# Performance work log

Hardware: AMD Instinct MI355X
Metric: run time of the kernel (lower is better)

Reference implementation:

```python
import jax, jax.numpy as jnp
import numpy as np

BETA = 5.0
NEG = jnp.float32(-1e30)  # finite stand-in for -inf; avoids NaN on the fully-masked row 0


def setup_inputs() -> dict:
    key = jax.random.key(0)
    ks = jax.random.split(key, 6)
    B, L, d, dv, dh = 4, 4096, 512, 512, 512
    K = jax.random.normal(ks[0], (B, L, d), dtype=jnp.float32)
    V = jax.random.normal(ks[1], (B, L, dv), dtype=jnp.float32)
    # nn.Linear weights: shape (out, in), applied as x @ W.T
    Wq = jax.random.normal(ks[2], (dh, d), dtype=jnp.float32) / np.sqrt(d).astype(np.float32)
    Wk = jax.random.normal(ks[3], (dh, d), dtype=jnp.float32) / np.sqrt(d).astype(np.float32)
    Wv = jax.random.normal(ks[4], (dv, dv), dtype=jnp.float32) / np.sqrt(dv).astype(np.float32)
    Wo = jax.random.normal(ks[5], (dv, dv), dtype=jnp.float32) / np.sqrt(dv).astype(np.float32)
    return {"K": K, "V": V, "Wq": Wq, "Wk": Wk, "Wv": Wv, "Wo": Wo}


def reference(K, V, Wq, Wk, Wv, Wo):
    B, L, _ = K.shape
    dh = Wq.shape[0]
    Qh = jnp.einsum('bld,hd->blh', K, Wq)
    Kh = jnp.einsum('bld,hd->blh', K, Wk)
    Vp = jnp.einsum('bld,ed->ble', V, Wv)
    scale = jnp.float32(BETA) / jnp.sqrt(jnp.float32(dh))
    scores = jnp.einsum('bih,bjh->bij', Qh, Kh) * scale  # [B,L,L]
    # strict causal mask: attend only to j <= i-1 (triu with diagonal=0 masked)
    mask = jnp.triu(jnp.ones((L, L), dtype=bool), k=0)
    scores = jnp.where(mask[None], NEG, scores)
    attn = jax.nn.softmax(scores, axis=-1)
    # row 0 has no past: torch code zeroes it after softmax
    attn = attn.at[:, 0, :].set(0.0)
    out = jnp.einsum('bij,bjd->bid', attn, Vp)
    Vhat = jnp.einsum('bld,ed->ble', out, Wo)
    return Vhat
```

## Files before the change

kernel.cpp:

```cpp
#include <hip/hip_runtime.h>


typedef unsigned short u16;
typedef _Float16 f16;
typedef short short8 __attribute__((ext_vector_type(8)));
typedef _Float16 half8 __attribute__((ext_vector_type(8)));
typedef _Float16 half4 __attribute__((ext_vector_type(4)));
typedef float floatx4 __attribute__((ext_vector_type(4)));

#define L_SEQ 4096
#define NBATCH 4
#define DMODEL 512
#define SCALE 0.22097086912079612f
#define MMAX 30.0f

__device__ __forceinline__ u16 f2bf(float f) {
  unsigned int u = __float_as_uint(f);
  u += 0x7fffu + ((u >> 16) & 1u);
  return (u16)(u >> 16);
}
__device__ __forceinline__ float bf2f(u16 h) {
  return __uint_as_float(((unsigned int)h) << 16);
}

__device__ __forceinline__ void gl2lds16(const void* g, void* l) {
  __builtin_amdgcn_global_load_lds(
      (const __attribute__((address_space(1))) unsigned int*)g,
      (__attribute__((address_space(3))) unsigned int*)l, 16, 0, 0);
}

__global__ __launch_bounds__(256) void cvt_f16v(const float4* __restrict__ x,
                                                half4* __restrict__ o, int n4) {
  int i = blockIdx.x * 256 + threadIdx.x;
  if (i >= n4) return;
  float4 f = x[i];
  half4 h = {(f16)f.x, (f16)f.y, (f16)f.z, (f16)f.w};
  o[i] = h;
}

template <int OUT_MODE>
__global__ __launch_bounds__(256, 2) void gemm128(
    const f16* __restrict__ A, const f16* __restrict__ B,
    void* __restrict__ Cout, int ldc, long sAz, long sBz, long sCz) {
  __shared__ f16 sA[128 * 64];
  __shared__ f16 sB[128 * 64];

  const int tid = threadIdx.x;
  const int wave = tid >> 6, lane = tid & 63, quad = lane >> 4, l16 = lane & 15;
  const int wm = (wave >> 1) * 64, wn = (wave & 1) * 64;
  const int bn = blockIdx.x * 128, bm = blockIdx.y * 128, bz = blockIdx.z;

  const f16* Ab = A + (long)bz * sAz + (long)bm * 512;
  const f16* Bb = B + (long)bz * sBz + (long)bn * 512;

  floatx4 zero = {0.f, 0.f, 0.f, 0.f};
  floatx4 acc[4][4];
#pragma unroll
  for (int mi = 0; mi < 4; mi++)
#pragma unroll
    for (int ni = 0; ni < 4; ni++) acc[mi][ni] = zero;

  const int lrow = lane >> 3;
  for (int ks = 0; ks < 8; ks++) {
    __syncthreads();
#pragma unroll
    for (int i = 0; i < 4; i++) {
      int r0 = wave * 32 + i * 8;
      int r = r0 + lrow;
      int c = ((lane & 7) - r) & 7;
      gl2lds16(Ab + (long)r * 512 + ks * 64 + c * 8, &sA[r0 * 64]);
      gl2lds16(Bb + (long)r * 512 + ks * 64 + c * 8, &sB[r0 * 64]);
    }
    __syncthreads();
#pragma unroll
    for (int kk = 0; kk < 2; kk++) {
      half8 af[4], bf[4];
#pragma unroll
      for (int mi = 0; mi < 4; mi++) {
        int row = wm + mi * 16 + l16;
        int slot = (kk * 4 + quad + row) & 7;
        af[mi] = *(const half8*)&sA[row * 64 + slot * 8];
      }
#pragma unroll
      for (int ni = 0; ni < 4; ni++) {
        int row = wn + ni * 16 + l16;
        int slot = (kk * 4 + quad + row) & 7;
        bf[ni] = *(const half8*)&sB[row * 64 + slot * 8];
      }
#pragma unroll
      for (int mi = 0; mi < 4; mi++)
#pragma unroll
        for (int ni = 0; ni < 4; ni++)
          acc[mi][ni] = __builtin_amdgcn_mfma_f32_16x16x32_f16(
              af[mi], bf[ni], acc[mi][ni], 0, 0, 0);
    }
  }

#pragma unroll
  for (int mi = 0; mi < 4; mi++) {
#pragma unroll
    for (int ni = 0; ni < 4; ni++) {
#pragma unroll
      for (int rr = 0; rr < 4; rr++) {
        int row = bm + wm + mi * 16 + quad * 4 + rr;
        int col = bn + wn + ni * 16 + l16;
        long idx = (long)bz * sCz + (long)row * ldc + col;
        float v = acc[mi][ni][rr];
        if (OUT_MODE == 1) {
          ((f16*)Cout)[idx] = (f16)v;
        } else if (OUT_MODE == 3) {
          ((u16*)Cout)[idx] = f2bf(v);
        } else {
          ((float*)Cout)[idx] = v;
        }
      }
    }
  }
}

__device__ __forceinline__ int nseg_of(int qt) {
  return (qt < 12) ? ((qt + 2) >> 1) : ((qt + 4) >> 2);
}
__device__ __forceinline__ int seg_off(int qt) {
  int o = 0;
  for (int q = 2; q < qt; q++) o += 4 * nseg_of(q);
  return o;
}

#define SV_LD 40

__global__ __launch_bounds__(512, 2) void attn_kernel(
    const f16* __restrict__ Qh_g, const f16* __restrict__ Kh_g,
    const u16* __restrict__ VpT, f16* __restrict__ Ob,
    u16* __restrict__ Opart, float* __restrict__ ml) {
  __shared__ f16 sK[2][32 * 512];
  __shared__ u16 sV[2][512 * 32];
  __shared__ u16 sP[8 * 16 * SV_LD];
  __shared__ float sL[128];

  const int tid = threadIdx.x;
  const int wave = tid >> 6, lane = tid & 63, quad = lane >> 4, l16 = lane & 15;

  int id = blockIdx.x;
  int qt = 31;
  for (;;) {
    int c = 4 * nseg_of(qt);
    if (id < c) break;
    id -= c;
    qt--;
  }
  const int S = nseg_of(qt);
  const int b = id / S;
  const int s = id - b * S;
  const int ktn = 4 * qt + 4;
  const int base = ktn / S, rem = ktn - base * S;
  const int len = base + (s < rem);
  const int start = s * base + (s < rem ? s : rem);

  const int q0 = qt * 128 + wave * 16;
  const long qbase = (long)b * L_SEQ + q0;

  half8 qf[16];
#pragma unroll
  for (int c = 0; c < 16; c++) {
    long a = (qbase + l16) * 512 + c * 32 + quad * 8;
    qf[c] = *(const half8*)&Qh_g[a];
  }

  floatx4 zero = {0.f, 0.f, 0.f, 0.f};
  float l_run[4] = {0.f, 0.f, 0.f, 0.f};
  floatx4 oacc[32];
#pragma unroll
  for (int nb = 0; nb < 32; nb++) oacc[nb] = zero;

  const f16* __restrict__ Kh_b = Kh_g + (long)b * L_SEQ * 512;
  const u16* __restrict__ V_b  = VpT + (long)b * (512L * L_SEQ);

  auto stage = [&](int bs, int jt) {
    const int j0 = jt * 32;
#pragma unroll
    for (int i = 0; i < 4; i++) {
      int r = wave * 4 + i;
      int k = (lane - (r & 7)) & 63;
      gl2lds16(Kh_b + (long)(j0 + r) * 512 + k * 8, &sK[bs][r * 512]);
    }
#pragma unroll
    for (int i = 0; i < 4; i++) {
      int g = wave * 4 + i;
      int d = g * 16 + (lane >> 2);
      int c = ((lane & 3) - d) & 3;
      gl2lds16(V_b + (long)d * L_SEQ + j0 + c * 8, &sV[bs][g * 512]);
    }
  };

  stage(0, start);

  for (int v = 0; v < len; v++) {
    const int j0 = (start + v) * 32;
    const int cur = v & 1;

    __syncthreads();
    if (v + 1 < len) stage(cur ^ 1, start + v + 1);

    const f16* kc = &sK[cur][0];
    const u16* vc = &sV[cur][0];

    floatx4 sacc0 = zero, sacc1 = zero;
    const int rot = l16 & 7;
#pragma unroll
    for (int c = 0; c < 16; c++) {
      int slot = (c * 4 + quad + rot) & 63;
      half8 b0 = *(const half8*)&kc[l16 * 512 + slot * 8];
      half8 b1 = *(const half8*)&kc[(16 + l16) * 512 + slot * 8];
      sacc0 = __builtin_amdgcn_mfma_f32_16x16x32_f16(qf[c], b0, sacc0, 0, 0, 0);
      sacc1 = __builtin_amdgcn_mfma_f32_16x16x32_f16(qf[c], b1, sacc1, 0, 0, 0);
    }

#pragma unroll
    for (int rr = 0; rr < 4; rr++) {
      int irow = q0 + quad * 4 + rr;
      float s0 = fmaf(sacc0[rr], SCALE, -MMAX);
      float s1 = fmaf(sacc1[rr], SCALE, -MMAX);
      if (j0 + l16 >= irow) s0 = -1e30f;
      if (j0 + 16 + l16 >= irow) s1 = -1e30f;
      float p0 = __expf(s0);
      float p1 = __expf(s1);
      l_run[rr] += p0 + p1;
      int pb = wave * (16 * SV_LD) + (quad * 4 + rr) * SV_LD;
      sP[pb + l16] = f2bf(p0);
      sP[pb + 16 + l16] = f2bf(p1);
    }

    __builtin_amdgcn_sched_barrier(0);
    __builtin_amdgcn_s_waitcnt(0xC07F);
    __builtin_amdgcn_s_barrier();
    __builtin_amdgcn_sched_barrier(0);

    short8 vf[4];
#pragma unroll
    for (int nbl = 0; nbl < 4; nbl++) {
      int dvr = wave * 64 + nbl * 16 + l16;
      vf[nbl] = *(const short8*)&vc[dvr * 32 + ((quad + l16) & 3) * 8];
    }
#pragma unroll
    for (int qg = 0; qg < 8; qg++) {
      short8 ap = *(const short8*)&sP[qg * (16 * SV_LD) + l16 * SV_LD + quad * 8];
#pragma unroll
      for (int nbl = 0; nbl < 4; nbl++)
        oacc[qg * 4 + nbl] =
            __builtin_amdgcn_mfma_f32_16x16x32_bf16(ap, vf[nbl], oacc[qg * 4 + nbl], 0, 0, 0);
    }
  }

#pragma unroll
  for (int rr = 0; rr < 4; rr++) {
    float l = l_run[rr];
    l += __shfl_xor(l, 1);
    l += __shfl_xor(l, 2);
    l += __shfl_xor(l, 4);
    l += __shfl_xor(l, 8);
    l_run[rr] = l;
  }
  if (l16 == 0) {
#pragma unroll
    for (int rr = 0; rr < 4; rr++) sL[wave * 16 + quad * 4 + rr] = l_run[rr];
  }
  __syncthreads();

  if (S == 1) {
#pragma unroll
    for (int qg = 0; qg < 8; qg++) {
#pragma unroll
      for (int rr = 0; rr < 4; rr++) {
        int row = qg * 16 + quad * 4 + rr;
        int irow = qt * 128 + row;
        float lv = sL[row];
        float inv = (irow == 0 || lv <= 0.f) ? 0.f : 1.0f / lv;
        long obase = ((long)b * L_SEQ + irow) * 512 + wave * 64;
#pragma unroll
        for (int nbl = 0; nbl < 4; nbl++)
          Ob[obase + nbl * 16 + l16] = (f16)(oacc[qg * 4 + nbl][rr] * inv);
      }
    }
  } else {
    const int slot = seg_off(qt) + b * S + s;
    const long obase0 = (long)slot * (128 * 512);
#pragma unroll
    for (int qg = 0; qg < 8; qg++) {
#pragma unroll
      for (int rr = 0; rr < 4; rr++) {
        int row = qg * 16 + quad * 4 + rr;
        long ob = obase0 + (long)row * 512 + wave * 64;
#pragma unroll
        for (int nbl = 0; nbl < 4; nbl++)
          Opart[ob + nbl * 16 + l16] = f2bf(oacc[qg * 4 + nbl][rr]);
      }
    }
    if (l16 == 0) {
#pragma unroll
      for (int rr = 0; rr < 4; rr++)
        ml[slot * 128 + wave * 16 + quad * 4 + rr] = l_run[rr];
    }
  }
}

__global__ __launch_bounds__(256) void attn_combine(
    const u16* __restrict__ Opart, const float* __restrict__ ml,
    f16* __restrict__ Ob) {
  const int qt = 2 + (blockIdx.x >> 2), b = blockIdx.x & 3;
  const int S = nseg_of(qt);
  const int bslot = seg_off(qt) + b * S;
  __shared__ float sInv[128];
  const int tid = threadIdx.x;
  if (tid < 128) {
    int row = tid, irow = qt * 128 + row;
    float ltot = 0.f;
    for (int s = 0; s < S; s++) ltot += ml[(bslot + s) * 128 + row];
    sInv[row] = (irow == 0 || ltot <= 0.f) ? 0.f : 1.0f / ltot;
  }
  __syncthreads();
  const int c0 = blockIdx.y * 16;
  for (int idx = tid; idx < 128 * 16; idx += 256) {
    int row = idx >> 4, cc = c0 + (idx & 15);
    float acc[8] = {0, 0, 0, 0, 0, 0, 0, 0};
    for (int s = 0; s < S; s++) {
      int4 pk = *(const int4*)&Opart[(long)(bslot + s) * 65536 + row * 512 + cc * 8];
      const u16* ph = (const u16*)&pk;
#pragma unroll
      for (int e = 0; e < 8; e++) acc[e] += bf2f(ph[e]);
    }
    float inv = sInv[row];
    f16 o[8];
#pragma unroll
    for (int e = 0; e < 8; e++) o[e] = (f16)(acc[e] * inv);
    *(int4*)&Ob[((long)b * L_SEQ + qt * 128 + row) * 512 + cc * 8] = *(int4*)o;
  }
}

extern "C" void kernel_launch(void* const* d_in, const int* in_sizes, int n_in,
                              void* d_out, int out_size, void* d_ws, size_t ws_size,
                              hipStream_t stream) {
  const float* K  = (const float*)d_in[0];
  const float* V  = (const float*)d_in[1];
  const float* Wq = (const float*)d_in[2];
  const float* Wk = (const float*)d_in[3];
  const float* Wv = (const float*)d_in[4];
  const float* Wo = (const float*)d_in[5];
  float* out = (float*)d_out;

  const int NKV = NBATCH * L_SEQ * DMODEL;
  const int NW = DMODEL * DMODEL;
  const int NSLOT = 640;

  char* w = (char*)d_ws;
  size_t off = 0;
  auto carve = [&](size_t bytes) {
    void* p = w + off;
    off += (bytes + 255) & ~(size_t)255;
    return p;
  };
  f16* Qh   = (f16*)carve((size_t)NKV * 2);
  f16* Kh   = (f16*)carve((size_t)NKV * 2);
  u16* VpTw = (u16*)carve((size_t)NKV * 2);
  f16* Obw  = (f16*)carve((size_t)NKV * 2);
  f16* Wo16 = (f16*)carve((size_t)NW * 2);
  float* mlw = (float*)carve((size_t)NSLOT * 128 * 4);
  u16* Opart = (u16*)carve((size_t)NSLOT * 65536 * 2);
  f16* K16  = (f16*)Opart;
  f16* V16  = K16 + NKV;
  f16* Wq16 = V16 + NKV;
  f16* Wk16 = Wq16 + NW;
  f16* Wv16 = Wk16 + NW;

  cvt_f16v<<<NKV / 1024, 256, 0, stream>>>((const float4*)K, (half4*)K16, NKV / 4);
  cvt_f16v<<<NKV / 1024, 256, 0, stream>>>((const float4*)V, (half4*)V16, NKV / 4);
  cvt_f16v<<<NW / 1024, 256, 0, stream>>>((const float4*)Wq, (half4*)Wq16, NW / 4);
  cvt_f16v<<<NW / 1024, 256, 0, stream>>>((const float4*)Wk, (half4*)Wk16, NW / 4);
  cvt_f16v<<<NW / 1024, 256, 0, stream>>>((const float4*)Wv, (half4*)Wv16, NW / 4);
  cvt_f16v<<<NW / 1024, 256, 0, stream>>>((const float4*)Wo, (half4*)Wo16, NW / 4);

  gemm128<1><<<dim3(4, 128, 1), 256, 0, stream>>>(
      K16, Wq16, (void*)Qh, 512, 0, 0, 0);
  gemm128<1><<<dim3(4, 128, 1), 256, 0, stream>>>(
      K16, Wk16, (void*)Kh, 512, 0, 0, 0);

  gemm128<3><<<dim3(32, 4, NBATCH), 256, 0, stream>>>(
      Wv16, V16, (void*)VpTw, L_SEQ, 0, (long)L_SEQ * 512, (long)512 * L_SEQ);

  attn_kernel<<<dim3(648, 1, 1), 512, 0, stream>>>(
      Qh, Kh, VpTw, Obw, Opart, mlw);
  attn_combine<<<dim3(120, 4, 1), 256, 0, stream>>>(Opart, mlw, Obw);

  gemm128<2><<<dim3(4, 128, 1), 256, 0, stream>>>(
      Obw, Wo16, (void*)out, 512, 0, 0, 0);

  (void)in_sizes; (void)n_in; (void)out_size; (void)ws_size;
}
```

Baseline: 358.2 us.

## Double KV tile to 64 and load V fragments directly from global

Widens the key tile from 32 to 64 rows per iteration, halving the number of barriers and loop trips per block. V is no longer staged through LDS; each wave loads its V fragments straight from global memory into registers, one half before the softmax and one half after the barrier. This frees LDS for the larger K double buffer but exposes global-load latency in the PV stage and raises register pressure, which may limit occupancy at two blocks per CU.

```diff
diff --git a/kernel.cpp b/kernel.cpp
--- a/kernel.cpp
+++ b/kernel.cpp
@@ -127,15 +127,14 @@
   return o;
 }
 
-#define SV_LD 40
+#define SP_LD 72
 
 __global__ __launch_bounds__(512, 2) void attn_kernel(
     const f16* __restrict__ Qh_g, const f16* __restrict__ Kh_g,
     const u16* __restrict__ VpT, f16* __restrict__ Ob,
     u16* __restrict__ Opart, float* __restrict__ ml) {
-  __shared__ f16 sK[2][32 * 512];
-  __shared__ u16 sV[2][512 * 32];
-  __shared__ u16 sP[8 * 16 * SV_LD];
+  __shared__ f16 sK[2][64 * 512];
+  __shared__ u16 sP[8 * 16 * SP_LD];
   __shared__ float sL[128];
 
   const int tid = threadIdx.x;
@@ -152,7 +151,7 @@
   const int S = nseg_of(qt);
   const int b = id / S;
   const int s = id - b * S;
-  const int ktn = 4 * qt + 4;
+  const int ktn = 2 * qt + 2;
   const int base = ktn / S, rem = ktn - base * S;
   const int len = base + (s < rem);
   const int start = s * base + (s < rem ? s : rem);
@@ -177,58 +176,59 @@
   const u16* __restrict__ V_b  = VpT + (long)b * (512L * L_SEQ);
 
   auto stage = [&](int bs, int jt) {
-    const int j0 = jt * 32;
-#pragma unroll
-    for (int i = 0; i < 4; i++) {
-      int r = wave * 4 + i;
+    const int j0 = jt * 64;
+#pragma unroll
+    for (int i = 0; i < 8; i++) {
+      int r = wave * 8 + i;
       int k = (lane - (r & 7)) & 63;
       gl2lds16(Kh_b + (long)(j0 + r) * 512 + k * 8, &sK[bs][r * 512]);
     }
-#pragma unroll
-    for (int i = 0; i < 4; i++) {
-      int g = wave * 4 + i;
-      int d = g * 16 + (lane >> 2);
-      int c = ((lane & 3) - d) & 3;
-      gl2lds16(V_b + (long)d * L_SEQ + j0 + c * 8, &sV[bs][g * 512]);
-    }
   };
 
   stage(0, start);
 
   for (int v = 0; v < len; v++) {
-    const int j0 = (start + v) * 32;
+    const int j0 = (start + v) * 64;
     const int cur = v & 1;
 
     __syncthreads();
     if (v + 1 < len) stage(cur ^ 1, start + v + 1);
 
     const f16* kc = &sK[cur][0];
-    const u16* vc = &sV[cur][0];
-
-    floatx4 sacc0 = zero, sacc1 = zero;
+
+    floatx4 sacc[4] = {zero, zero, zero, zero};
     const int rot = l16 & 7;
 #pragma unroll
     for (int c = 0; c < 16; c++) {
       int slot = (c * 4 + quad + rot) & 63;
-      half8 b0 = *(const half8*)&kc[l16 * 512 + slot * 8];
-      half8 b1 = *(const half8*)&kc[(16 + l16) * 512 + slot * 8];
-      sacc0 = __builtin_amdgcn_mfma_f32_16x16x32_f16(qf[c], b0, sacc0, 0, 0, 0);
-      sacc1 = __builtin_amdgcn_mfma_f32_16x16x32_f16(qf[c], b1, sacc1, 0, 0, 0);
+#pragma unroll
+      for (int t = 0; t < 4; t++) {
+        half8 bt = *(const half8*)&kc[(t * 16 + l16) * 512 + slot * 8];
+        sacc[t] = __builtin_amdgcn_mfma_f32_16x16x32_f16(qf[c], bt, sacc[t], 0, 0, 0);
+      }
+    }
+
+    short8 vf0[4];
+#pragma unroll
+    for (int nbl = 0; nbl < 4; nbl++) {
+      long dvr = wave * 64 + nbl * 16 + l16;
+      vf0[nbl] = *(const short8*)&V_b[dvr * L_SEQ + j0 + quad * 8];
     }
 
 #pragma unroll
     for (int rr = 0; rr < 4; rr++) {
       int irow = q0 + quad * 4 + rr;
-      float s0 = fmaf(sacc0[rr], SCALE, -MMAX);
-      float s1 = fmaf(sacc1[rr], SCALE, -MMAX);
-      if (j0 + l16 >= irow) s0 = -1e30f;
-      if (j0 + 16 + l16 >= irow) s1 = -1e30f;
-      float p0 = __expf(s0);
-      float p1 = __expf(s1);
-      l_run[rr] += p0 + p1;
-      int pb = wave * (16 * SV_LD) + (quad * 4 + rr) * SV_LD;
-      sP[pb + l16] = f2bf(p0);
-      sP[pb + 16 + l16] = f2bf(p1);
+      int pb = wave * (16 * SP_LD) + (quad * 4 + rr) * SP_LD;
+      float lacc = 0.f;
+#pragma unroll
+      for (int t = 0; t < 4; t++) {
+        float st = fmaf(sacc[t][rr], SCALE, -MMAX);
+        if (j0 + t * 16 + l16 >= irow) st = -1e30f;
+        float p = __expf(st);
+        lacc += p;
+        sP[pb + t * 16 + l16] = f2bf(p);
+      }
+      l_run[rr] += lacc;
     }
 
     __builtin_amdgcn_sched_barrier(0);
@@ -236,19 +236,27 @@
     __builtin_amdgcn_s_barrier();
     __builtin_amdgcn_sched_barrier(0);
 
-    short8 vf[4];
+    short8 vf1[4];
 #pragma unroll
     for (int nbl = 0; nbl < 4; nbl++) {
-      int dvr = wave * 64 + nbl * 16 + l16;
-      vf[nbl] = *(const short8*)&vc[dvr * 32 + ((quad + l16) & 3) * 8];
+      long dvr = wave * 64 + nbl * 16 + l16;
+      vf1[nbl] = *(const short8*)&V_b[dvr * L_SEQ + j0 + 32 + quad * 8];
     }
 #pragma unroll
     for (int qg = 0; qg < 8; qg++) {
-      short8 ap = *(const short8*)&sP[qg * (16 * SV_LD) + l16 * SV_LD + quad * 8];
+      short8 ap = *(const short8*)&sP[qg * (16 * SP_LD) + l16 * SP_LD + quad * 8];
 #pragma unroll
       for (int nbl = 0; nbl < 4; nbl++)
         oacc[qg * 4 + nbl] =
-            __builtin_amdgcn_mfma_f32_16x16x32_bf16(ap, vf[nbl], oacc[qg * 4 + nbl], 0, 0, 0);
+            __builtin_amdgcn_mfma_f32_16x16x32_bf16(ap, vf0[nbl], oacc[qg * 4 + nbl], 0, 0, 0);
+    }
+#pragma unroll
+    for (int qg = 0; qg < 8; qg++) {
+      short8 ap = *(const short8*)&sP[qg * (16 * SP_LD) + l16 * SP_LD + 32 + quad * 8];
+#pragma unroll
+      for (int nbl = 0; nbl < 4; nbl++)
+        oacc[qg * 4 + nbl] =
+            __builtin_amdgcn_mfma_f32_16x16x32_bf16(ap, vf1[nbl], oacc[qg * 4 + nbl], 0, 0, 0);
     }
   }
 
```

New measurement: 404.4 us. +12.9%, slower.
